# Kernel optimization log

Measured on AMD Instinct MI355X. Metric: run time of the kernel, lower is better.

Reference implementation:

```python
import jax, jax.numpy as jnp
import numpy as np

NUM_HEADS = 8
NVIEW = 5
EPS = 1e-6


def setup_inputs() -> dict:
    key = jax.random.key(0)
    k1, k2, k3 = jax.random.split(key, 3)
    BV, HW, C = 20, 4096, 256
    x = jax.random.normal(k1, (BV, HW, C), dtype=jnp.float32)
    # torch.nn.Linear default init ~ U(-1/sqrt(in), 1/sqrt(in)); scale randn similarly
    W_qkv = jax.random.normal(k2, (C, 3 * C), dtype=jnp.float32) * (1.0 / np.sqrt(C))
    W_proj = jax.random.normal(k3, (C, C), dtype=jnp.float32) * (1.0 / np.sqrt(C))
    b_proj = jnp.zeros((C,), dtype=jnp.float32)
    return {"x": x, "W_qkv": W_qkv, "W_proj": W_proj, "b_proj": b_proj}


def reference(x, W_qkv, W_proj, b_proj):
    BV, HW, C = x.shape
    V = NVIEW
    B = BV // V
    H = NUM_HEADS
    d = C // H
    L = V * HW

    # merge views into one long sequence per batch element
    xb = x.reshape(B, L, C)

    # qkv projection (qkv_bias=False) -> [B, L, 3, H, d]
    qkv = (xb @ W_qkv).reshape(B, L, 3, H, d)
    q = qkv[:, :, 0]  # [B, L, H, d]
    k = qkv[:, :, 1]
    v = qkv[:, :, 2]

    # elu + 1 feature map, computed in float32 (as in the autocast-disabled block)
    q = (jax.nn.elu(q) + 1.0).astype(jnp.float32)
    k = (jax.nn.elu(k) + 1.0).astype(jnp.float32)
    v = v.astype(jnp.float32)

    # linear attention: kv = sum_l k_l (x) v_l  -> [B, H, m, d]
    kv = jnp.einsum('nlhd,nlhm->nhmd', k, v)
    # normalizer z = 1 / (q . sum_l k_l)  -> [B, L, H]
    k_sum = k.sum(axis=1)  # [B, H, d]
    z = 1.0 / (jnp.einsum('nlhd,nhd->nlh', q, k_sum) + EPS)
    # output y -> [B, L, H, m]
    y = jnp.einsum('nlhd,nhmd,nlh->nlhm', q, kv, z)

    y = y.reshape(BV, HW, C)
    return y @ W_proj + b_proj
```

## Files before the change

### kernel.cpp

```cpp
#include <hip/hip_runtime.h>

#define M_ROWS 81920
#define KDIM 256
#define NQKV 768
#define LROWS 20480
#define EPSV 1e-6f

using bf16x8 = __attribute__((ext_vector_type(8))) short;
using f32x4  = __attribute__((ext_vector_type(4))) float;

static __device__ __forceinline__ unsigned short f2bf(float f) {
  union { float f; unsigned int u; } c; c.f = f;
  unsigned int u = c.u;
  u += 0x7fff + ((u >> 16) & 1);
  return (unsigned short)(u >> 16);
}
static __device__ __forceinline__ float bf2f(unsigned short h) {
  union { unsigned int u; float f; } c; c.u = ((unsigned int)h) << 16;
  return c.f;
}

static __device__ __forceinline__ void async_cp16(const void* g, void* l) {
  __builtin_amdgcn_global_load_lds(
      (const __attribute__((address_space(1))) void*)(unsigned long long)g,
      (__attribute__((address_space(3))) void*)(unsigned int)(unsigned long long)l,
      16, 0, 0);
}

__global__ void cvt_x(const float* __restrict__ x, unsigned short* __restrict__ xb) {
  long i = ((long)blockIdx.x * blockDim.x + threadIdx.x) * 4;
  float4 v = *(const float4*)(x + i);
  ushort4 o;
  o.x = f2bf(v.x); o.y = f2bf(v.y); o.z = f2bf(v.z); o.w = f2bf(v.w);
  *(ushort4*)(xb + i) = o;
}

__global__ void transpose_w(const float* __restrict__ w, unsigned short* __restrict__ wt,
                            int K, int N) {
  int k = blockIdx.x;
  for (int n = threadIdx.x; n < N; n += blockDim.x)
    wt[(size_t)n * K + k] = f2bf(w[(size_t)k * N + n]);
}

template <int EPI>
__global__ __launch_bounds__(256, 3)
void gemm_bt(const unsigned short* __restrict__ A,
             const unsigned short* __restrict__ Bt,
             void* __restrict__ C,
             const float* __restrict__ bias,
             int N) {
  __shared__ unsigned short As[128 * 32];
  __shared__ unsigned short Bs[128 * 32];
  const int K = 256;
  int t = threadIdx.x;
  int lane = t & 63;
  int w = t >> 6;
  int m0 = blockIdx.y * 128;
  int n0 = blockIdx.x * 128;
  const unsigned short* Bp = Bt;
  if (EPI == 1) Bp += (size_t)(blockIdx.y / 160) * 256 * 256;

  f32x4 acc[4][4];
#pragma unroll
  for (int i = 0; i < 4; i++)
#pragma unroll
    for (int j = 0; j < 4; j++) acc[i][j] = (f32x4){0.f, 0.f, 0.f, 0.f};

  int wm = w & 1, wn = w >> 1;
  int fm = lane & 15;
  int fk = (lane >> 4) * 8;
  int r0a = t >> 2, p0 = t & 3;
  int r1a = (t + 256) >> 2, p1 = t & 3;

  for (int kt = 0; kt < 8; kt++) {
    int k0 = kt * 32;
    __syncthreads();
    async_cp16(A + (size_t)(m0 + r0a) * K + k0 + p0 * 8, As + (size_t)t * 8);
    async_cp16(A + (size_t)(m0 + r1a) * K + k0 + p1 * 8, As + (size_t)(t + 256) * 8);
    async_cp16(Bp + (size_t)(n0 + r0a) * K + k0 + p0 * 8, Bs + (size_t)t * 8);
    async_cp16(Bp + (size_t)(n0 + r1a) * K + k0 + p1 * 8, Bs + (size_t)(t + 256) * 8);
    __syncthreads();
    bf16x8 af[4], bfr[4];
#pragma unroll
    for (int i = 0; i < 4; i++)
      af[i] = *(const bf16x8*)(As + (wm * 64 + i * 16 + fm) * 32 + fk);
#pragma unroll
    for (int j = 0; j < 4; j++)
      bfr[j] = *(const bf16x8*)(Bs + (wn * 64 + j * 16 + fm) * 32 + fk);
#pragma unroll
    for (int i = 0; i < 4; i++)
#pragma unroll
      for (int j = 0; j < 4; j++)
        acc[i][j] = __builtin_amdgcn_mfma_f32_16x16x32_bf16(af[i], bfr[j], acc[i][j], 0, 0, 0);
  }

  int quad = lane >> 4;
  int col = lane & 15;
#pragma unroll
  for (int i = 0; i < 4; i++) {
#pragma unroll
    for (int j = 0; j < 4; j++) {
      int gm_base = m0 + wm * 64 + i * 16 + quad * 4;
      int gn = n0 + wn * 64 + j * 16 + col;
#pragma unroll
      for (int r = 0; r < 4; r++) {
        float v = acc[i][j][r];
        int gm = gm_base + r;
        if (EPI == 0) {
          if (gn < 512) v = (v > 0.f) ? v + 1.f : __expf(v);
          ((unsigned short*)C)[(size_t)gm * N + gn] = f2bf(v);
        } else {
          ((float*)C)[(size_t)gm * N + gn] = v + bias[gn];
        }
      }
    }
  }
}

__global__ __launch_bounds__(256)
void kv_reduce(const unsigned short* __restrict__ qkv, float* __restrict__ kv,
               float* __restrict__ ksum) {
  __shared__ unsigned short s[64 * 64];
  int pair = blockIdx.x;
  int n = pair >> 3, h = pair & 7;
  int chunk = blockIdx.y;
  const int RC = LROWS / 16;
  int r0 = n * LROWS + chunk * RC;
  int t = threadIdx.x;
  int lane = t & 63;
  int w = t >> 6;

  float accv[4][4] = {};
  float ks[4] = {};
  int mg = lane >> 3;
  int m0 = mg * 4, d0 = (lane & 7) * 4;

  int row0 = t >> 3, part0 = t & 7;
  int row1 = (t + 256) >> 3, part1 = t & 7;

  for (int tile = 0; tile < RC / 64; tile++) {
    __syncthreads();
    {
      size_t gr = (size_t)(r0 + tile * 64 + row0) * 768;
      const unsigned short* g = (part0 < 4) ? (qkv + gr + 256 + h * 32 + part0 * 8)
                                            : (qkv + gr + 512 + h * 32 + (part0 - 4) * 8);
      async_cp16(g, s + (size_t)t * 8);
      gr = (size_t)(r0 + tile * 64 + row1) * 768;
      g = (part1 < 4) ? (qkv + gr + 256 + h * 32 + part1 * 8)
                      : (qkv + gr + 512 + h * 32 + (part1 - 4) * 8);
      async_cp16(g, s + (size_t)(t + 256) * 8);
    }
    __syncthreads();
    for (int rr = 0; rr < 16; rr++) {
      int row = w * 16 + rr;
      ushort4 kk = *(const ushort4*)(s + row * 64 + d0);
      ushort4 vv = *(const ushort4*)(s + row * 64 + 32 + m0);
      float kf[4] = {bf2f(kk.x), bf2f(kk.y), bf2f(kk.z), bf2f(kk.w)};
      float vf[4] = {bf2f(vv.x), bf2f(vv.y), bf2f(vv.z), bf2f(vv.w)};
#pragma unroll
      for (int i = 0; i < 4; i++)
#pragma unroll
        for (int j = 0; j < 4; j++) accv[i][j] += vf[i] * kf[j];
      if (mg == 0) {
        ks[0] += kf[0]; ks[1] += kf[1]; ks[2] += kf[2]; ks[3] += kf[3];
      }
    }
  }
  float* base = kv + (size_t)pair * 1024;
#pragma unroll
  for (int i = 0; i < 4; i++)
#pragma unroll
    for (int j = 0; j < 4; j++) atomicAdd(base + (m0 + i) * 32 + (d0 + j), accv[i][j]);
  if (mg == 0) {
    float* kb = ksum + pair * 32;
#pragma unroll
    for (int j = 0; j < 4; j++) atomicAdd(kb + d0 + j, ks[j]);
  }
}

__global__ __launch_bounds__(256)
void make_g(const float* __restrict__ kv, const float* __restrict__ wproj,
            unsigned short* __restrict__ gt) {
  __shared__ float kvs[1024];
  int pair = blockIdx.x;
  int n = pair >> 3, h = pair & 7;
  int c = threadIdx.x;
  for (int i = c; i < 1024; i += 256) kvs[i] = kv[(size_t)pair * 1024 + i];
  __syncthreads();
  float acc[32];
#pragma unroll
  for (int d = 0; d < 32; d++) acc[d] = 0.f;
  for (int m = 0; m < 32; m++) {
    float wp = wproj[(size_t)(h * 32 + m) * 256 + c];
#pragma unroll
    for (int d = 0; d < 32; d++) acc[d] += kvs[m * 32 + d] * wp;
  }
  unsigned short* o = gt + ((size_t)n * 256 + c) * 256 + h * 32;
#pragma unroll
  for (int d = 0; d < 32; d++) o[d] = f2bf(acc[d]);
}

__global__ __launch_bounds__(256)
void scale_q(const unsigned short* __restrict__ qkv, const float* __restrict__ ksum,
             unsigned short* __restrict__ qp) {
  int t = threadIdx.x;
  int lane32 = t & 31;
  int rsub = t >> 5;
  long r0 = (long)blockIdx.x * 64;
  for (int p = 0; p < 8; p++) {
    long r = r0 + p * 8 + rsub;
    int n = (int)(r / LROWS);
    const unsigned short* q = qkv + r * 768 + lane32 * 8;
    ushort4 a = *(const ushort4*)(q);
    ushort4 b = *(const ushort4*)(q + 4);
    float qf[8] = {bf2f(a.x), bf2f(a.y), bf2f(a.z), bf2f(a.w),
                   bf2f(b.x), bf2f(b.y), bf2f(b.z), bf2f(b.w)};
    const float* ks = ksum + n * 256 + lane32 * 8;
    float sacc = 0.f;
#pragma unroll
    for (int i = 0; i < 8; i++) sacc += qf[i] * ks[i];
    sacc += __shfl_xor(sacc, 1);
    sacc += __shfl_xor(sacc, 2);
    float z = 1.f / (sacc + EPSV);
    ushort4 oa, ob;
    oa.x = f2bf(qf[0] * z); oa.y = f2bf(qf[1] * z);
    oa.z = f2bf(qf[2] * z); oa.w = f2bf(qf[3] * z);
    ob.x = f2bf(qf[4] * z); ob.y = f2bf(qf[5] * z);
    ob.z = f2bf(qf[6] * z); ob.w = f2bf(qf[7] * z);
    unsigned short* o = qp + r * 256 + lane32 * 8;
    *(ushort4*)o = oa;
    *(ushort4*)(o + 4) = ob;
  }
}

extern "C" void kernel_launch(void* const* d_in, const int* in_sizes, int n_in,
                              void* d_out, int out_size, void* d_ws, size_t ws_size,
                              hipStream_t stream) {
  (void)in_sizes; (void)n_in; (void)out_size; (void)ws_size;
  const float* x = (const float*)d_in[0];
  const float* Wqkv = (const float*)d_in[1];
  const float* Wproj = (const float*)d_in[2];
  const float* bproj = (const float*)d_in[3];
  float* out = (float*)d_out;

  char* ws = (char*)d_ws;
  unsigned short* xbf    = (unsigned short*)(ws);
  unsigned short* wqkvt  = (unsigned short*)(ws + 41943040);
  unsigned short* qkv_bf = (unsigned short*)(ws + 42336256);
  float*          kv     = (float*)(ws + 168165376);
  float*          ksum   = (float*)(ws + 168296448);
  unsigned short* gt     = (unsigned short*)(ws + 168300544);
  unsigned short* qp     = (unsigned short*)(ws + 168824832);

  hipMemsetAsync(kv, 0, 131072 + 4096, stream);

  cvt_x<<<M_ROWS * KDIM / 1024, 256, 0, stream>>>(x, xbf);
  transpose_w<<<256, 256, 0, stream>>>(Wqkv, wqkvt, 256, 768);
  gemm_bt<0><<<dim3(NQKV / 128, M_ROWS / 128), 256, 0, stream>>>(xbf, wqkvt, qkv_bf, nullptr, NQKV);
  kv_reduce<<<dim3(32, 16), 256, 0, stream>>>(qkv_bf, kv, ksum);
  make_g<<<32, 256, 0, stream>>>(kv, Wproj, gt);
  scale_q<<<M_ROWS / 64, 256, 0, stream>>>(qkv_bf, ksum, qp);
  gemm_bt<1><<<dim3(2, M_ROWS / 128), 256, 0, stream>>>(qp, gt, out, bproj, 256);
}
```

Before: 339.1 us.

## Restructure kv reduction into per-chunk partials plus a separate combine kernel

The kv/ksum reduction previously ran 512 blocks, each loading a narrow 64-byte k/v slice for one head and combining results with global float atomics after a zeroing memset. It now runs 640 blocks of 512 threads, each reading full contiguous 128-row k/v rows for all 8 heads (one wave per head) and writing partial sums to scratch in the reused x-bf16 workspace. A new combine kernel then sums the 160 partials per (batch, head), which removes the atomics and the memset. The cost is an extra launch and about 21 MB of partial writes and re-reads, with the combine running on only 32 blocks.

```diff
diff --git a/kernel.cpp b/kernel.cpp
--- a/kernel.cpp
+++ b/kernel.cpp
@@ -5,6 +5,7 @@
 #define NQKV 768
 #define LROWS 20480
 #define EPSV 1e-6f
+#define KV_CHUNKS 160
 
 using bf16x8 = __attribute__((ext_vector_type(8))) short;
 using f32x4  = __attribute__((ext_vector_type(4))) float;
@@ -117,65 +118,73 @@
   }
 }
 
-__global__ __launch_bounds__(256)
-void kv_reduce(const unsigned short* __restrict__ qkv, float* __restrict__ kv,
-               float* __restrict__ ksum) {
-  __shared__ unsigned short s[64 * 64];
-  int pair = blockIdx.x;
-  int n = pair >> 3, h = pair & 7;
-  int chunk = blockIdx.y;
-  const int RC = LROWS / 16;
-  int r0 = n * LROWS + chunk * RC;
+__global__ __launch_bounds__(512)
+void kv_reduce(const unsigned short* __restrict__ qkv, float* __restrict__ kvp) {
+  __shared__ unsigned short s[32 * 512];
+  int chunk = blockIdx.x;
+  int n = blockIdx.y;
   int t = threadIdx.x;
   int lane = t & 63;
   int w = t >> 6;
-
-  float accv[4][4] = {};
+  long r0 = (long)n * LROWS + (long)chunk * 128;
+
+  float acc[4][4] = {};
   float ks[4] = {};
   int mg = lane >> 3;
   int m0 = mg * 4, d0 = (lane & 7) * 4;
 
-  int row0 = t >> 3, part0 = t & 7;
-  int row1 = (t + 256) >> 3, part1 = t & 7;
-
-  for (int tile = 0; tile < RC / 64; tile++) {
-    __syncthreads();
-    {
-      size_t gr = (size_t)(r0 + tile * 64 + row0) * 768;
-      const unsigned short* g = (part0 < 4) ? (qkv + gr + 256 + h * 32 + part0 * 8)
-                                            : (qkv + gr + 512 + h * 32 + (part0 - 4) * 8);
-      async_cp16(g, s + (size_t)t * 8);
-      gr = (size_t)(r0 + tile * 64 + row1) * 768;
-      g = (part1 < 4) ? (qkv + gr + 256 + h * 32 + part1 * 8)
-                      : (qkv + gr + 512 + h * 32 + (part1 - 4) * 8);
-      async_cp16(g, s + (size_t)(t + 256) * 8);
+  for (int tile = 0; tile < 4; tile++) {
+    __syncthreads();
+#pragma unroll
+    for (int q = 0; q < 4; q++) {
+      int c = t + q * 512;
+      int row = c >> 6, part = c & 63;
+      async_cp16(qkv + (size_t)(r0 + tile * 32 + row) * 768 + 256 + part * 8,
+                 s + (size_t)c * 8);
     }
     __syncthreads();
-    for (int rr = 0; rr < 16; rr++) {
-      int row = w * 16 + rr;
-      ushort4 kk = *(const ushort4*)(s + row * 64 + d0);
-      ushort4 vv = *(const ushort4*)(s + row * 64 + 32 + m0);
+#pragma unroll 4
+    for (int row = 0; row < 32; row++) {
+      ushort4 kk = *(const ushort4*)(s + row * 512 + w * 32 + d0);
+      ushort4 vv = *(const ushort4*)(s + row * 512 + 256 + w * 32 + m0);
       float kf[4] = {bf2f(kk.x), bf2f(kk.y), bf2f(kk.z), bf2f(kk.w)};
       float vf[4] = {bf2f(vv.x), bf2f(vv.y), bf2f(vv.z), bf2f(vv.w)};
 #pragma unroll
       for (int i = 0; i < 4; i++)
 #pragma unroll
-        for (int j = 0; j < 4; j++) accv[i][j] += vf[i] * kf[j];
+        for (int j = 0; j < 4; j++) acc[i][j] += vf[i] * kf[j];
       if (mg == 0) {
         ks[0] += kf[0]; ks[1] += kf[1]; ks[2] += kf[2]; ks[3] += kf[3];
       }
     }
   }
-  float* base = kv + (size_t)pair * 1024;
+  float* o = kvp + ((size_t)(n * KV_CHUNKS + chunk) * 8 + w) * 1056;
 #pragma unroll
   for (int i = 0; i < 4; i++)
 #pragma unroll
-    for (int j = 0; j < 4; j++) atomicAdd(base + (m0 + i) * 32 + (d0 + j), accv[i][j]);
+    for (int j = 0; j < 4; j++) o[(m0 + i) * 32 + d0 + j] = acc[i][j];
   if (mg == 0) {
-    float* kb = ksum + pair * 32;
-#pragma unroll
-    for (int j = 0; j < 4; j++) atomicAdd(kb + d0 + j, ks[j]);
-  }
+#pragma unroll
+    for (int j = 0; j < 4; j++) o[1024 + d0 + j] = ks[j];
+  }
+}
+
+__global__ __launch_bounds__(256)
+void kv_combine(const float* __restrict__ kvp, float* __restrict__ kv,
+                float* __restrict__ ksum) {
+  int pair = blockIdx.x;
+  int n = pair >> 3, h = pair & 7;
+  int t = threadIdx.x;
+  float a0 = 0.f, a1 = 0.f, a2 = 0.f, a3 = 0.f, a4 = 0.f;
+  const float* base = kvp + ((size_t)(n * KV_CHUNKS) * 8 + h) * 1056;
+  for (int c = 0; c < KV_CHUNKS; c++) {
+    const float* p = base + (size_t)c * 8 * 1056;
+    a0 += p[t]; a1 += p[t + 256]; a2 += p[t + 512]; a3 += p[t + 768];
+    if (t < 32) a4 += p[1024 + t];
+  }
+  float* kvo = kv + (size_t)pair * 1024;
+  kvo[t] = a0; kvo[t + 256] = a1; kvo[t + 512] = a2; kvo[t + 768] = a3;
+  if (t < 32) ksum[pair * 32 + t] = a4;
 }
 
 __global__ __launch_bounds__(256)
@@ -245,6 +254,7 @@
 
   char* ws = (char*)d_ws;
   unsigned short* xbf    = (unsigned short*)(ws);
+  float*          kvp    = (float*)(ws);
   unsigned short* wqkvt  = (unsigned short*)(ws + 41943040);
   unsigned short* qkv_bf = (unsigned short*)(ws + 42336256);
   float*          kv     = (float*)(ws + 168165376);
@@ -252,12 +262,11 @@
   unsigned short* gt     = (unsigned short*)(ws + 168300544);
   unsigned short* qp     = (unsigned short*)(ws + 168824832);
 
-  hipMemsetAsync(kv, 0, 131072 + 4096, stream);
-
   cvt_x<<<M_ROWS * KDIM / 1024, 256, 0, stream>>>(x, xbf);
   transpose_w<<<256, 256, 0, stream>>>(Wqkv, wqkvt, 256, 768);
   gemm_bt<0><<<dim3(NQKV / 128, M_ROWS / 128), 256, 0, stream>>>(xbf, wqkvt, qkv_bf, nullptr, NQKV);
-  kv_reduce<<<dim3(32, 16), 256, 0, stream>>>(qkv_bf, kv, ksum);
+  kv_reduce<<<dim3(KV_CHUNKS, 4), 512, 0, stream>>>(qkv_bf, kvp);
+  kv_combine<<<32, 256, 0, stream>>>(kvp, kv, ksum);
   make_g<<<32, 256, 0, stream>>>(kv, Wproj, gt);
   scale_q<<<M_ROWS / 64, 256, 0, stream>>>(qkv_bf, ksum, qp);
   gemm_bt<1><<<dim3(2, M_ROWS / 128), 256, 0, stream>>>(qp, gt, out, bproj, 256);
```

New measurement: 350.3 us. 3.3% more time.
